# Optimization experiments

Measured on AMD Instinct MI355X. Metric: run time of the kernel, lower is better.

## Reference

```python
import jax, jax.numpy as jnp
import numpy as np
import math

DIM = 1024
HEADS = 16
DIM_HEAD = 64
INNER = HEADS * DIM_HEAD
NUM_BUCKETS = 32
MAX_DISTANCE = 128


def _relative_position_bucket(rel_pos, num_buckets=NUM_BUCKETS, max_distance=MAX_DISTANCE):
    # Faithful to torch version: n = -relative_position, buckets halved for sign.
    n = -rel_pos
    num_buckets = num_buckets // 2  # 16
    ret = (n < 0).astype(jnp.int32) * num_buckets
    n = jnp.abs(n)
    max_exact = num_buckets // 2  # 8
    is_small = n < max_exact
    # guard log(0); masked out by is_small anyway
    val_if_large = max_exact + (
        jnp.log(jnp.maximum(n, 1).astype(jnp.float32) / max_exact)
        / math.log(max_distance / max_exact) * (num_buckets - max_exact)
    ).astype(jnp.int32)  # .long() truncation (values >= 0 so trunc == floor)
    val_if_large = jnp.minimum(val_if_large, num_buckets - 1)
    return ret + jnp.where(is_small, n, val_if_large)


def _rel_bias(rel_emb, n):
    pos = jnp.arange(n, dtype=jnp.int32)
    rel = pos[None, :] - pos[:, None]          # (i, j): k_pos - q_pos
    bucket = _relative_position_bucket(rel)    # (n, n) int32
    vals = rel_emb[bucket]                     # (n, n, h)
    return jnp.transpose(vals, (2, 0, 1))      # (h, n, n)


def setup_inputs() -> dict:
    key = jax.random.key(0)
    ks = jax.random.split(key, 6)
    x = jax.random.normal(ks[0], (2, 2048, DIM), dtype=jnp.float32)
    # linear weights stored (in, out); torch Linear math y = x @ W.T is equivalent
    Wq = jax.random.normal(ks[1], (DIM, INNER), dtype=jnp.float32) * (DIM ** -0.5)
    Wkv = jax.random.normal(ks[2], (DIM, 2 * INNER), dtype=jnp.float32) * (DIM ** -0.5)
    Wo = jax.random.normal(ks[3], (INNER, DIM), dtype=jnp.float32) * (INNER ** -0.5)
    bo = jax.random.normal(ks[4], (DIM,), dtype=jnp.float32) * 0.01
    rel_emb = jax.random.normal(ks[5], (NUM_BUCKETS, HEADS), dtype=jnp.float32)
    return {"x": x, "Wq": Wq, "Wkv": Wkv, "Wo": Wo, "bo": bo, "rel_emb": rel_emb}


def reference(x, Wq, Wkv, Wo, bo, rel_emb):
    b, n, _ = x.shape
    h, d = HEADS, DIM_HEAD
    scale = d ** -0.5
    q = (x @ Wq).reshape(b, n, h, d).transpose(0, 2, 1, 3)          # (b,h,n,d)
    kv = x @ Wkv                                                     # (b,n,2*inner)
    k, v = jnp.split(kv, 2, axis=-1)
    k = k.reshape(b, n, h, d).transpose(0, 2, 1, 3)
    v = v.reshape(b, n, h, d).transpose(0, 2, 1, 3)
    dots = jnp.einsum('bhid,bhjd->bhij', q, k) * scale               # (b,h,n,n)
    dots = dots + _rel_bias(rel_emb, n)[None]                        # add T5 bias
    attn = jax.nn.softmax(dots, axis=-1)
    out = jnp.einsum('bhij,bhjd->bhid', attn, v)                     # (b,h,n,d)
    out = out.transpose(0, 2, 1, 3).reshape(b, n, h * d)             # (b,n,inner)
    return out @ Wo + bo
```

## Files before the change

### kernel.cpp

```cpp
#include <hip/hip_runtime.h>

typedef unsigned short u16;
typedef __attribute__((ext_vector_type(8))) __bf16 bf16x8;
typedef __attribute__((ext_vector_type(4))) float f32x4;

#define MFMA16(a, b, c) __builtin_amdgcn_mfma_f32_16x16x32_bf16((a), (b), (c), 0, 0, 0)

__device__ __forceinline__ u16 f2bf(float f) {
  union { float f; unsigned u; } c; c.f = f;
  unsigned u = c.u;
  u += 0x7FFFu + ((u >> 16) & 1u);
  return (u16)(u >> 16);
}

__device__ __forceinline__ bf16x8 pack8(const float4& a, const float4& b) {
  union { u16 u[8]; bf16x8 v; } r;
  r.u[0] = f2bf(a.x); r.u[1] = f2bf(a.y); r.u[2] = f2bf(a.z); r.u[3] = f2bf(a.w);
  r.u[4] = f2bf(b.x); r.u[5] = f2bf(b.y); r.u[6] = f2bf(b.z); r.u[7] = f2bf(b.w);
  return r.v;
}

__device__ __forceinline__ void async_cp16(u16* l, const u16* g) {
  __builtin_amdgcn_global_load_lds(
      (const __attribute__((address_space(1))) unsigned int*)g,
      (__attribute__((address_space(3))) unsigned int*)l, 16, 0, 0);
}

__global__ __launch_bounds__(256) void transpose_all_k(
    const float* __restrict__ Wq, const float* __restrict__ Wkv,
    const float* __restrict__ Wo, u16* __restrict__ Wall,
    u16* __restrict__ WoT) {
  __shared__ u16 t[32][33];
  const int z = blockIdx.z;
  const float* src; u16* dst; int C_ld, col0;
  if (z == 0)      { src = Wo;  dst = WoT;                C_ld = 1024; col0 = 0; }
  else if (z == 1) { src = Wq;  dst = Wall;               C_ld = 1024; col0 = 0; }
  else if (z == 2) { src = Wkv; dst = Wall + 1024 * 1024; C_ld = 2048; col0 = 0; }
  else             { src = Wkv; dst = Wall + 2048 * 1024; C_ld = 2048; col0 = 1024; }
  const int bx = blockIdx.x * 32;
  const int by = blockIdx.y * 32;
  const int tx = threadIdx.x;
  for (int yo = threadIdx.y; yo < 32; yo += 8)
    t[yo][tx] = f2bf(src[(size_t)(by + yo) * C_ld + col0 + bx + tx]);
  __syncthreads();
  for (int yo = threadIdx.y; yo < 32; yo += 8)
    dst[(size_t)(bx + yo) * 1024 + by + tx] = t[tx][yo];
}

__global__ void bias_table_k(const float* __restrict__ rel_emb, float* __restrict__ tab) {
  int idx = blockIdx.x * blockDim.x + threadIdx.x;
  if (idx >= 4095) return;
  int delta = idx - 2047;
  int n = -delta;
  int ret = 0;
  if (n < 0) { ret = 16; n = -n; }
  int bucket;
  if (n < 8) {
    bucket = n;
  } else {
    int vl = 8 + (int)(2.0f * __log2f((float)n * 0.125f));
    bucket = vl < 15 ? vl : 15;
  }
  bucket += ret;
#pragma unroll
  for (int h = 0; h < 16; h++)
    tab[(size_t)idx * 16 + h] = rel_emb[bucket * 16 + h];
}

__global__ __launch_bounds__(256) void proj_gemm_k(
    const float* __restrict__ Xf, const u16* __restrict__ WT,
    u16* __restrict__ dstQ, u16* __restrict__ dstK, u16* __restrict__ dstVT) {
  __shared__ __align__(16) u16 As[128 * 32];
  __shared__ __align__(16) u16 Bs[128 * 32];
  f32x4 acc[4][4];
#pragma unroll
  for (int i = 0; i < 4; i++)
#pragma unroll
    for (int j = 0; j < 4; j++) acc[i][j] = f32x4{0.f, 0.f, 0.f, 0.f};

  const int m0 = blockIdx.x * 128;
  const int n0 = blockIdx.y * 128;
  const int tid  = threadIdx.x;
  const int lane = tid & 63;
  const int wave = tid >> 6;
  const int wr = (wave >> 1) * 64;
  const int wc = (wave & 1) * 64;
  const int lr = lane & 15;
  const int lk = (lane >> 4) * 8;
  const int r0 = tid >> 2;
  const int sg = (tid & 3) * 8;

  const float* ap0 = Xf + (size_t)(m0 + r0) * 1024 + sg;
  const float* ap1 = Xf + (size_t)(m0 + 64 + r0) * 1024 + sg;
  const u16* bp0 = WT + (size_t)(n0 + r0) * 1024 + sg;
  const u16* bp1 = WT + (size_t)(n0 + 64 + r0) * 1024 + sg;
  u16* as0 = As + r0 * 32 + sg;
  u16* as1 = As + (64 + r0) * 32 + sg;
  u16* bs0 = Bs + r0 * 32 + sg;
  u16* bs1 = Bs + (64 + r0) * 32 + sg;

  for (int k0 = 0; k0 < 1024; k0 += 32) {
    __syncthreads();
    async_cp16(bs0, bp0 + k0);
    async_cp16(bs1, bp1 + k0);
    float4 a00 = *(const float4*)(ap0 + k0);
    float4 a01 = *(const float4*)(ap0 + k0 + 4);
    float4 a10 = *(const float4*)(ap1 + k0);
    float4 a11 = *(const float4*)(ap1 + k0 + 4);
    *(bf16x8*)as0 = pack8(a00, a01);
    *(bf16x8*)as1 = pack8(a10, a11);
    __syncthreads();
    bf16x8 af[4], bfv[4];
#pragma unroll
    for (int i = 0; i < 4; i++)
      af[i] = *(const bf16x8*)(As + (wr + i * 16 + lr) * 32 + lk);
#pragma unroll
    for (int j = 0; j < 4; j++)
      bfv[j] = *(const bf16x8*)(Bs + (wc + j * 16 + lr) * 32 + lk);
#pragma unroll
    for (int i = 0; i < 4; i++)
#pragma unroll
      for (int j = 0; j < 4; j++)
        acc[i][j] = MFMA16(af[i], bfv[j], acc[i][j]);
  }

  const int orow = (lane >> 4) * 4, ocol = lane & 15;
#pragma unroll
  for (int i = 0; i < 4; i++)
#pragma unroll
    for (int j = 0; j < 4; j++)
#pragma unroll
      for (int r = 0; r < 4; r++) {
        int grow = m0 + wr + i * 16 + orow + r;
        int gcol = n0 + wc + j * 16 + ocol;
        int b = grow >> 11, n = grow & 2047;
        int seg = gcol >> 10;
        int c = gcol & 1023;
        int h = c >> 6, d = c & 63;
        u16 bv = f2bf(acc[i][j][r]);
        if (seg == 0)
          dstQ[(((size_t)b * 16 + h) * 2048 + n) * 64 + d] = bv;
        else if (seg == 1)
          dstK[(((size_t)b * 16 + h) * 2048 + n) * 64 + d] = bv;
        else
          dstVT[(((size_t)b * 16 + h) * 64 + d) * 2048 + n] = bv;
      }
}

__global__ __launch_bounds__(256) void attn_k(
    const u16* __restrict__ Q, const u16* __restrict__ Kb,
    const u16* __restrict__ VT, const float* __restrict__ bias_tab,
    u16* __restrict__ AO) {
  const int tid = threadIdx.x;
  const int lane = tid & 63, wave = tid >> 6;
  const int lr = lane & 15, lq = lane >> 4, lk = lq * 8;
  const int bh = blockIdx.y, b = bh >> 4, h = bh & 15;
  const int q0 = blockIdx.x * 64;

  __shared__ __align__(16) u16 Qs[64 * 72];
  __shared__ __align__(16) u16 Ks[64 * 72];
  __shared__ __align__(16) u16 Vs[64 * 72];
  __shared__ float Bls[128];
  u16* Ps = Qs;

  const u16* Qg = Q + ((size_t)bh * 2048 + q0) * 64;
  {
    int ra = tid >> 3, sa = (tid & 7) * 8;
    *(bf16x8*)(Qs + ra * 72 + sa)        = *(const bf16x8*)(Qg + (size_t)ra * 64 + sa);
    *(bf16x8*)(Qs + (32 + ra) * 72 + sa) = *(const bf16x8*)(Qg + (size_t)(32 + ra) * 64 + sa);
  }
  __syncthreads();
  bf16x8 qf0 = *(const bf16x8*)(Qs + (wave * 16 + lr) * 72 + lk);
  bf16x8 qf1 = *(const bf16x8*)(Qs + (wave * 16 + lr) * 72 + 32 + lk);

  float m_run[4], l_run[4];
  f32x4 o[4];
#pragma unroll
  for (int r = 0; r < 4; r++) { m_run[r] = -1.0e30f; l_run[r] = 0.f; }
#pragma unroll
  for (int dt = 0; dt < 4; dt++) o[dt] = f32x4{0.f, 0.f, 0.f, 0.f};

  const u16* Kg = Kb + (size_t)bh * 2048 * 64;
  const u16* Vg = VT + (size_t)bh * 64 * 2048;
  const int i_base = wave * 16 + lq * 4;
  const float scale = 0.125f;

  for (int kc = 0; kc < 2048; kc += 64) {
    __syncthreads();
    {
      int ra = tid >> 3, sa = (tid & 7) * 8;
      *(bf16x8*)(Ks + ra * 72 + sa)        = *(const bf16x8*)(Kg + (size_t)(kc + ra) * 64 + sa);
      *(bf16x8*)(Ks + (32 + ra) * 72 + sa) = *(const bf16x8*)(Kg + (size_t)(kc + 32 + ra) * 64 + sa);
      *(bf16x8*)(Vs + ra * 72 + sa)        = *(const bf16x8*)(Vg + (size_t)ra * 2048 + kc + sa);
      *(bf16x8*)(Vs + (32 + ra) * 72 + sa) = *(const bf16x8*)(Vg + (size_t)(32 + ra) * 2048 + kc + sa);
      if (tid < 127) Bls[tid] = bias_tab[(size_t)(kc - q0 + tid - 63 + 2047) * 16 + h];
    }
    __syncthreads();

    f32x4 sc[4];
#pragma unroll
    for (int jt = 0; jt < 4; jt++) {
      bf16x8 kb0 = *(const bf16x8*)(Ks + (jt * 16 + lr) * 72 + lk);
      bf16x8 kb1 = *(const bf16x8*)(Ks + (jt * 16 + lr) * 72 + 32 + lk);
      f32x4 z = {0.f, 0.f, 0.f, 0.f};
      z = MFMA16(qf0, kb0, z);
      z = MFMA16(qf1, kb1, z);
      sc[jt] = z;
    }

    float mc[4] = {-1.0e30f, -1.0e30f, -1.0e30f, -1.0e30f};
#pragma unroll
    for (int jt = 0; jt < 4; jt++) {
      int base = jt * 16 + lr - i_base + 63;
#pragma unroll
      for (int r = 0; r < 4; r++) {
        float sv = sc[jt][r] * scale + Bls[base - r];
        sc[jt][r] = sv;
        mc[r] = fmaxf(mc[r], sv);
      }
    }
#pragma unroll
    for (int m = 1; m < 16; m <<= 1)
#pragma unroll
      for (int r = 0; r < 4; r++)
        mc[r] = fmaxf(mc[r], __shfl_xor(mc[r], m));

    float alpha[4], ls[4];
#pragma unroll
    for (int r = 0; r < 4; r++) {
      float mn = fmaxf(m_run[r], mc[r]);
      alpha[r] = __expf(m_run[r] - mn);
      m_run[r] = mn;
      ls[r] = 0.f;
    }
#pragma unroll
    for (int jt = 0; jt < 4; jt++)
#pragma unroll
      for (int r = 0; r < 4; r++) {
        float p = __expf(sc[jt][r] - m_run[r]);
        sc[jt][r] = p;
        ls[r] += p;
      }
#pragma unroll
    for (int m = 1; m < 16; m <<= 1)
#pragma unroll
      for (int r = 0; r < 4; r++)
        ls[r] += __shfl_xor(ls[r], m);
#pragma unroll
    for (int r = 0; r < 4; r++)
      l_run[r] = l_run[r] * alpha[r] + ls[r];
#pragma unroll
    for (int dt = 0; dt < 4; dt++)
#pragma unroll
      for (int r = 0; r < 4; r++)
        o[dt][r] *= alpha[r];

#pragma unroll
    for (int jt = 0; jt < 4; jt++)
#pragma unroll
      for (int r = 0; r < 4; r++)
        Ps[(wave * 16 + lq * 4 + r) * 72 + jt * 16 + lr] = f2bf(sc[jt][r]);
    __syncthreads();

    bf16x8 p0 = *(const bf16x8*)(Ps + (wave * 16 + lr) * 72 + lk);
    bf16x8 p1 = *(const bf16x8*)(Ps + (wave * 16 + lr) * 72 + 32 + lk);
#pragma unroll
    for (int dt = 0; dt < 4; dt++) {
      bf16x8 v0 = *(const bf16x8*)(Vs + (dt * 16 + lr) * 72 + lk);
      bf16x8 v1 = *(const bf16x8*)(Vs + (dt * 16 + lr) * 72 + 32 + lk);
      o[dt] = MFMA16(p0, v0, o[dt]);
      o[dt] = MFMA16(p1, v1, o[dt]);
    }
  }

#pragma unroll
  for (int dt = 0; dt < 4; dt++)
#pragma unroll
    for (int r = 0; r < 4; r++) {
      float ov = o[dt][r] / l_run[r];
      int n = q0 + wave * 16 + lq * 4 + r;
      int d = dt * 16 + lr;
      AO[((size_t)b * 2048 + n) * 1024 + h * 64 + d] = f2bf(ov);
    }
}

__global__ __launch_bounds__(256) void out_gemm_k(
    const u16* __restrict__ AO, const u16* __restrict__ WoT,
    const float* __restrict__ bo, float* __restrict__ out) {
  __shared__ __align__(16) u16 As[64 * 32];
  __shared__ __align__(16) u16 Bs[128 * 32];
  f32x4 acc[4][2];
#pragma unroll
  for (int i = 0; i < 4; i++)
#pragma unroll
    for (int j = 0; j < 2; j++) acc[i][j] = f32x4{0.f, 0.f, 0.f, 0.f};

  const int m0 = blockIdx.x * 64;
  const int n0 = blockIdx.y * 128;
  const int tid  = threadIdx.x;
  const int lane = tid & 63;
  const int wave = tid >> 6;
  const int wc = wave * 32;
  const int lr = lane & 15;
  const int lk = (lane >> 4) * 8;
  const int r0 = tid >> 2;
  const int sg = (tid & 3) * 8;

  const u16* ap  = AO + (size_t)(m0 + r0) * 1024 + sg;
  const u16* bp0 = WoT + (size_t)(n0 + r0) * 1024 + sg;
  const u16* bp1 = WoT + (size_t)(n0 + 64 + r0) * 1024 + sg;
  u16* as  = As + r0 * 32 + sg;
  u16* bs0 = Bs + r0 * 32 + sg;
  u16* bs1 = Bs + (64 + r0) * 32 + sg;

  for (int k0 = 0; k0 < 1024; k0 += 32) {
    __syncthreads();
    async_cp16(as,  ap  + k0);
    async_cp16(bs0, bp0 + k0);
    async_cp16(bs1, bp1 + k0);
    __syncthreads();
    bf16x8 af[4], bfv[2];
#pragma unroll
    for (int i = 0; i < 4; i++)
      af[i] = *(const bf16x8*)(As + (i * 16 + lr) * 32 + lk);
#pragma unroll
    for (int j = 0; j < 2; j++)
      bfv[j] = *(const bf16x8*)(Bs + (wc + j * 16 + lr) * 32 + lk);
#pragma unroll
    for (int i = 0; i < 4; i++)
#pragma unroll
      for (int j = 0; j < 2; j++)
        acc[i][j] = MFMA16(af[i], bfv[j], acc[i][j]);
  }

  const int orow = (lane >> 4) * 4, ocol = lane & 15;
#pragma unroll
  for (int i = 0; i < 4; i++)
#pragma unroll
    for (int j = 0; j < 2; j++) {
      int gcol = n0 + wc + j * 16 + ocol;
      float bof = bo[gcol];
#pragma unroll
      for (int r = 0; r < 4; r++) {
        int grow = m0 + i * 16 + orow + r;
        out[(size_t)grow * 1024 + gcol] = acc[i][j][r] + bof;
      }
    }
}

extern "C" void kernel_launch(void* const* d_in, const int* in_sizes, int n_in,
                              void* d_out, int out_size, void* d_ws, size_t ws_size,
                              hipStream_t stream) {
  const float* x    = (const float*)d_in[0];
  const float* Wq   = (const float*)d_in[1];
  const float* Wkv  = (const float*)d_in[2];
  const float* Wo   = (const float*)d_in[3];
  const float* bo   = (const float*)d_in[4];
  const float* rel  = (const float*)d_in[5];
  float* out = (float*)d_out;

  char* ws = (char*)d_ws;
  u16*   WoT  = (u16*)(ws + 0);
  float* btab = (float*)(ws + 2097152);
  u16*   Qb   = (u16*)(ws + 2359296);
  u16*   Kbuf = (u16*)(ws + 10747904);
  u16*   VTb  = (u16*)(ws + 19136512);
  u16*   AO   = (u16*)(ws + 27525120);
  u16*   Wall = AO;

  bias_table_k<<<16, 256, 0, stream>>>(rel, btab);
  transpose_all_k<<<dim3(32, 32, 4), dim3(32, 8), 0, stream>>>(Wq, Wkv, Wo, Wall, WoT);

  proj_gemm_k<<<dim3(32, 24), 256, 0, stream>>>(x, Wall, Qb, Kbuf, VTb);

  attn_k<<<dim3(32, 32), 256, 0, stream>>>(Qb, Kbuf, VTb, btab, AO);
  out_gemm_k<<<dim3(64, 8), 256, 0, stream>>>(AO, WoT, bo, out);
}
```

Measured before the change: 300.9 us.

## Double-buffer LDS tiles in projection and output GEMMs to overlap loads

Both GEMM kernels now keep two LDS buffers per operand. The next K tile is prefetched (async global-to-LDS copies for B, register loads then bf16 packing for A in proj) while MFMAs run on the current tile, which cuts one barrier per iteration. The goal is to hide global load latency behind compute. It doubles LDS use, which may lower occupancy, and relies on the single barrier per iteration to be enough for the async LDS writes.

```diff
diff --git a/kernel.cpp b/kernel.cpp
--- a/kernel.cpp
+++ b/kernel.cpp
@@ -70,8 +70,8 @@
 __global__ __launch_bounds__(256) void proj_gemm_k(
     const float* __restrict__ Xf, const u16* __restrict__ WT,
     u16* __restrict__ dstQ, u16* __restrict__ dstK, u16* __restrict__ dstVT) {
-  __shared__ __align__(16) u16 As[128 * 32];
-  __shared__ __align__(16) u16 Bs[128 * 32];
+  __shared__ __align__(16) u16 As[2][128 * 32];
+  __shared__ __align__(16) u16 Bs[2][128 * 32];
   f32x4 acc[4][4];
 #pragma unroll
   for (int i = 0; i < 4; i++)
@@ -94,34 +94,54 @@
   const float* ap1 = Xf + (size_t)(m0 + 64 + r0) * 1024 + sg;
   const u16* bp0 = WT + (size_t)(n0 + r0) * 1024 + sg;
   const u16* bp1 = WT + (size_t)(n0 + 64 + r0) * 1024 + sg;
-  u16* as0 = As + r0 * 32 + sg;
-  u16* as1 = As + (64 + r0) * 32 + sg;
-  u16* bs0 = Bs + r0 * 32 + sg;
-  u16* bs1 = Bs + (64 + r0) * 32 + sg;
-
+  const int ao0 = r0 * 32 + sg;
+  const int ao1 = (64 + r0) * 32 + sg;
+  const int bo0 = ao0, bo1 = ao1;
+
+  async_cp16(&Bs[0][bo0], bp0);
+  async_cp16(&Bs[0][bo1], bp1);
+  {
+    float4 a00 = *(const float4*)(ap0);
+    float4 a01 = *(const float4*)(ap0 + 4);
+    float4 a10 = *(const float4*)(ap1);
+    float4 a11 = *(const float4*)(ap1 + 4);
+    *(bf16x8*)&As[0][ao0] = pack8(a00, a01);
+    *(bf16x8*)&As[0][ao1] = pack8(a10, a11);
+  }
+  __syncthreads();
+
+  int cur = 0;
   for (int k0 = 0; k0 < 1024; k0 += 32) {
-    __syncthreads();
-    async_cp16(bs0, bp0 + k0);
-    async_cp16(bs1, bp1 + k0);
-    float4 a00 = *(const float4*)(ap0 + k0);
-    float4 a01 = *(const float4*)(ap0 + k0 + 4);
-    float4 a10 = *(const float4*)(ap1 + k0);
-    float4 a11 = *(const float4*)(ap1 + k0 + 4);
-    *(bf16x8*)as0 = pack8(a00, a01);
-    *(bf16x8*)as1 = pack8(a10, a11);
-    __syncthreads();
+    const int nxt = cur ^ 1;
+    const int kn = k0 + 32;
+    const bool have_next = (kn < 1024);
+    float4 a00, a01, a10, a11;
+    if (have_next) {
+      async_cp16(&Bs[nxt][bo0], bp0 + kn);
+      async_cp16(&Bs[nxt][bo1], bp1 + kn);
+      a00 = *(const float4*)(ap0 + kn);
+      a01 = *(const float4*)(ap0 + kn + 4);
+      a10 = *(const float4*)(ap1 + kn);
+      a11 = *(const float4*)(ap1 + kn + 4);
+    }
     bf16x8 af[4], bfv[4];
 #pragma unroll
     for (int i = 0; i < 4; i++)
-      af[i] = *(const bf16x8*)(As + (wr + i * 16 + lr) * 32 + lk);
+      af[i] = *(const bf16x8*)&As[cur][(wr + i * 16 + lr) * 32 + lk];
 #pragma unroll
     for (int j = 0; j < 4; j++)
-      bfv[j] = *(const bf16x8*)(Bs + (wc + j * 16 + lr) * 32 + lk);
+      bfv[j] = *(const bf16x8*)&Bs[cur][(wc + j * 16 + lr) * 32 + lk];
 #pragma unroll
     for (int i = 0; i < 4; i++)
 #pragma unroll
       for (int j = 0; j < 4; j++)
         acc[i][j] = MFMA16(af[i], bfv[j], acc[i][j]);
+    if (have_next) {
+      *(bf16x8*)&As[nxt][ao0] = pack8(a00, a01);
+      *(bf16x8*)&As[nxt][ao1] = pack8(a10, a11);
+    }
+    __syncthreads();
+    cur = nxt;
   }
 
   const int orow = (lane >> 4) * 4, ocol = lane & 15;
@@ -287,8 +307,8 @@
 __global__ __launch_bounds__(256) void out_gemm_k(
     const u16* __restrict__ AO, const u16* __restrict__ WoT,
     const float* __restrict__ bo, float* __restrict__ out) {
-  __shared__ __align__(16) u16 As[64 * 32];
-  __shared__ __align__(16) u16 Bs[128 * 32];
+  __shared__ __align__(16) u16 As[2][64 * 32];
+  __shared__ __align__(16) u16 Bs[2][128 * 32];
   f32x4 acc[4][2];
 #pragma unroll
   for (int i = 0; i < 4; i++)
@@ -309,28 +329,39 @@
   const u16* ap  = AO + (size_t)(m0 + r0) * 1024 + sg;
   const u16* bp0 = WoT + (size_t)(n0 + r0) * 1024 + sg;
   const u16* bp1 = WoT + (size_t)(n0 + 64 + r0) * 1024 + sg;
-  u16* as  = As + r0 * 32 + sg;
-  u16* bs0 = Bs + r0 * 32 + sg;
-  u16* bs1 = Bs + (64 + r0) * 32 + sg;
-
+  const int ao  = r0 * 32 + sg;
+  const int bo0 = r0 * 32 + sg;
+  const int bo1 = (64 + r0) * 32 + sg;
+
+  async_cp16(&As[0][ao],  ap);
+  async_cp16(&Bs[0][bo0], bp0);
+  async_cp16(&Bs[0][bo1], bp1);
+  __syncthreads();
+
+  int cur = 0;
   for (int k0 = 0; k0 < 1024; k0 += 32) {
-    __syncthreads();
-    async_cp16(as,  ap  + k0);
-    async_cp16(bs0, bp0 + k0);
-    async_cp16(bs1, bp1 + k0);
-    __syncthreads();
+    const int nxt = cur ^ 1;
+    const int kn = k0 + 32;
+    const bool have_next = (kn < 1024);
+    if (have_next) {
+      async_cp16(&As[nxt][ao],  ap  + kn);
+      async_cp16(&Bs[nxt][bo0], bp0 + kn);
+      async_cp16(&Bs[nxt][bo1], bp1 + kn);
+    }
     bf16x8 af[4], bfv[2];
 #pragma unroll
     for (int i = 0; i < 4; i++)
-      af[i] = *(const bf16x8*)(As + (i * 16 + lr) * 32 + lk);
+      af[i] = *(const bf16x8*)&As[cur][(i * 16 + lr) * 32 + lk];
 #pragma unroll
     for (int j = 0; j < 2; j++)
-      bfv[j] = *(const bf16x8*)(Bs + (wc + j * 16 + lr) * 32 + lk);
+      bfv[j] = *(const bf16x8*)&Bs[cur][(wc + j * 16 + lr) * 32 + lk];
 #pragma unroll
     for (int i = 0; i < 4; i++)
 #pragma unroll
       for (int j = 0; j < 2; j++)
         acc[i][j] = MFMA16(af[i], bfv[j], acc[i][j]);
+    __syncthreads();
+    cur = nxt;
   }
 
   const int orow = (lane >> 4) * 4, ocol = lane & 15;
```

After: 303.0 us. No clear change (+0.7%).
